# Kernel optimization log

Measured on AMD Instinct MI355X. Metric: run time of the kernel, lower is better.

## Reference

```python
import jax, jax.numpy as jnp
import numpy as np

BG_ID = 0
RADIUS = 10
MODE = 'gauss'
LAMBDA_B = 1.0
GAMMA = 0.1
TEMP = 4.0
EPS = 1e-8
BIG = 1e6  # stands in for +inf (no fg in a row/column); BIG**2 is fp32-safe


def setup_inputs() -> dict:
    key = jax.random.key(0)
    k1, k2 = jax.random.split(key)
    B, C, H, W = 4, 19, 256, 256
    return {
        'student_logits': jax.random.normal(k1, (B, C, H, W), jnp.float32),
        'teacher_logits': jax.random.normal(k2, (B, C, H, W), jnp.float32),
    }


def _edt2(fg):
    """Exact squared Euclidean distance transform of (1 - fg):
    distance from each pixel to the nearest foreground pixel.
    Separable algorithm: 1D column pass (two cumulative scans), then
    exact lower-envelope minimization along rows (vectorized brute force).
    fg: bool [B, H, W]. Returns float32 [B, H, W]."""
    B, H, W = fg.shape
    ii = jnp.arange(H, dtype=jnp.float32)[None, :, None]  # row index
    # 1D vertical distance to nearest fg pixel in each column
    d_fwd = ii - jax.lax.cummax(jnp.where(fg, ii, -BIG), axis=1)
    d_bwd = -jax.lax.cummax(jnp.where(fg, -ii, -BIG), axis=1, reverse=True) - ii
    g = jnp.minimum(jnp.minimum(d_fwd, d_bwd), BIG)  # [B,H,W]
    # exact 2D squared EDT: dist2[b,i,j] = min_{j'} (j-j')^2 + g[b,i,j']^2
    jj = jnp.arange(W, dtype=jnp.float32)
    diff2 = (jj[:, None] - jj[None, :]) ** 2  # [W, W']
    dist2 = jnp.min(diff2[None, None, :, :] + (g * g)[:, :, None, :], axis=-1)
    return dist2


def _erode(fg):
    """scipy.ndimage.binary_erosion with 4-connected cross structure and
    border_value=0 (out-of-bounds treated as background)."""
    p = jnp.pad(fg, ((0, 0), (1, 1), (1, 1)))
    return fg & p[:, :-2, 1:-1] & p[:, 2:, 1:-1] & p[:, 1:-1, :-2] & p[:, 1:-1, 2:]


def _weight_map(teacher_logits):
    # argmax of softmax(probs) == argmax of logits (softmax is monotone per-pixel)
    pred = jnp.argmax(teacher_logits, axis=1)  # [B,H,W]
    fg = pred != BG_ID
    dist2 = _edt2(fg)
    dist = jnp.sqrt(dist2)
    mask = (dist <= RADIUS).astype(jnp.float32)
    sigma = RADIUS / 2.0
    if MODE == 'gauss':
        wdist = jnp.exp(-dist2 / (2.0 * sigma * sigma))
    else:
        wdist = jnp.clip(1.0 - dist / RADIUS, 0.0, 1.0)
    wdist = wdist * mask
    boundary = (fg & ~_erode(fg)).astype(jnp.float32)
    # wb = wdist*(1+lambda_b*boundary); final weights = wb*mask_inside
    # (if an image has no fg pixels, dist is huge -> mask==0 -> weights==0,
    #  matching the scipy loop's `continue` which leaves zeros)
    return wdist * (1.0 + LAMBDA_B * boundary) * mask


def reference(student_logits, teacher_logits):
    weight_map = _weight_map(teacher_logits)  # [B,H,W]
    # teacher probs at temperature T (torch computes t_prob_T and t_prob
    # identically twice; computed once here)
    t_prob = jax.nn.softmax(teacher_logits / TEMP, axis=1)
    entropy = -jnp.sum(t_prob * jnp.log(jnp.clip(t_prob, EPS, None)), axis=1)
    ent_max = jnp.max(entropy, axis=(1, 2), keepdims=True)
    conf_factor = GAMMA + (1.0 - GAMMA) * (1.0 - entropy / (ent_max + EPS))
    s_logp = jax.nn.log_softmax(student_logits / TEMP, axis=1)
    kl_per_pixel = jnp.sum(t_prob * (jnp.log(t_prob + EPS) - s_logp), axis=1)
    total_weight = weight_map * conf_factor
    loss = jnp.sum(total_weight * kl_per_pixel) / (jnp.sum(total_weight) + EPS)
    return TEMP * TEMP * loss
```

## Files before the change

kernel.cpp:

```cpp
#include <hip/hip_runtime.h>
#include <math.h>

#define NC   19
#define HH   256
#define WW   256
#define NB   4
#define HW   (HH * WW)
#define NPIX (NB * HW)
#define RAD  10
#define CAP2 121.0f

__global__ __launch_bounds__(256) void k_pixel(
    const float* __restrict__ student, const float* __restrict__ teacher,
    float* __restrict__ entropy, float* __restrict__ kl,
    unsigned char* __restrict__ fg, float* __restrict__ bmax,
    double* __restrict__ acc, unsigned int* __restrict__ done)
{
    if (blockIdx.x == 0 && threadIdx.x == 0) {
        acc[0] = 0.0; acc[1] = 0.0; *done = 0u;
    }
    int q = (blockIdx.x * 256 + threadIdx.x) * 2;
    int b = q >> 16;
    int r = q & (HW - 1);
    const float* tb = teacher + (size_t)b * NC * HW + r;
    const float* sb = student + (size_t)b * NC * HW + r;

    float2 t[NC], s[NC];
    float tmx = -INFINITY, tmy = -INFINITY, smx = -INFINITY, smy = -INFINITY;
    int ax = 0, ay = 0;
#pragma unroll
    for (int c = 0; c < NC; ++c) {
        t[c] = *(const float2*)(tb + (size_t)c * HW);
        s[c] = *(const float2*)(sb + (size_t)c * HW);
        if (t[c].x > tmx) { tmx = t[c].x; ax = c; }
        if (t[c].y > tmy) { tmy = t[c].y; ay = c; }
        smx = fmaxf(smx, s[c].x);
        smy = fmaxf(smy, s[c].y);
    }
    float Stx = 0.f, Sty = 0.f, Ssx = 0.f, Ssy = 0.f;
    float T1x = 0.f, T1y = 0.f, T2x = 0.f, T2y = 0.f;
#pragma unroll
    for (int c = 0; c < NC; ++c) {
        float ex = __expf((t[c].x - tmx) * 0.25f);
        float ey = __expf((t[c].y - tmy) * 0.25f);
        Stx += ex;            Sty += ey;
        T1x += ex * t[c].x;   T1y += ey * t[c].y;
        T2x += ex * s[c].x;   T2y += ey * s[c].y;
        Ssx += __expf((s[c].x - smx) * 0.25f);
        Ssy += __expf((s[c].y - smy) * 0.25f);
    }
    float rStx = 1.0f / Stx, rSty = 1.0f / Sty;
    float entx = (tmx - T1x * rStx) * 0.25f + __logf(Stx);
    float enty = (tmy - T1y * rSty) * 0.25f + __logf(Sty);
    float klx = -entx - ((T2x * rStx - smx) * 0.25f - __logf(Ssx));
    float kly = -enty - ((T2y * rSty - smy) * 0.25f - __logf(Ssy));

    *(float2*)(entropy + q) = make_float2(entx, enty);
    *(float2*)(kl + q)      = make_float2(klx, kly);
    uchar2 fgv = make_uchar2((ax != 0) ? 1 : 0, (ay != 0) ? 1 : 0);
    *(uchar2*)(fg + q) = fgv;

    float m = fmaxf(entx, enty);
#pragma unroll
    for (int o = 32; o >= 1; o >>= 1) m = fmaxf(m, __shfl_down(m, o, 64));
    __shared__ float smem[4];
    int wave = threadIdx.x >> 6, lane = threadIdx.x & 63;
    if (lane == 0) smem[wave] = m;
    __syncthreads();
    if (threadIdx.x == 0)
        bmax[blockIdx.x] = fmaxf(fmaxf(smem[0], smem[1]), fmaxf(smem[2], smem[3]));
}

#define TS   32
#define HALO 10
#define FW   (TS + 2 * HALO)

__global__ __launch_bounds__(256) void k_tile(
    const unsigned char* __restrict__ fg, const float* __restrict__ entropy,
    const float* __restrict__ kl, const float* __restrict__ bmax,
    double* __restrict__ acc, unsigned int* __restrict__ done,
    float* __restrict__ out)
{
    __shared__ float fgt[FW][FW];
    __shared__ float vm[TS][FW];
    __shared__ float wmax[4];
    int b   = blockIdx.z;
    int ti0 = blockIdx.y * TS;
    int tj0 = blockIdx.x * TS;
    int tid = threadIdx.x;
    int wave = tid >> 6, lane = tid & 63;
    const unsigned char* fgb = fg + (size_t)b * HW;

    float m = bmax[b * 128 + (tid & 127)];
#pragma unroll
    for (int o = 32; o >= 1; o >>= 1) m = fmaxf(m, __shfl_down(m, o, 64));
    if (lane == 0) wmax[wave] = m;

    for (int l = tid; l < FW * FW; l += 256) {
        int li = l / FW, lj = l - li * FW;
        int gi = ti0 - HALO + li, gj = tj0 - HALO + lj;
        float v = 0.f;
        if (gi >= 0 && gi < HH && gj >= 0 && gj < WW) v = (float)fgb[gi * WW + gj];
        fgt[li][lj] = v;
    }
    __syncthreads();
    float em = fmaxf(fmaxf(wmax[0], wmax[1]), fmaxf(wmax[2], wmax[3]));

    for (int l = tid; l < TS * FW; l += 256) {
        int i = l / FW, j = l - i * FW;
        float mn = CAP2;
#pragma unroll
        for (int di = -HALO; di <= HALO; ++di) {
            float fv = fgt[i + HALO + di][j];
            mn = fminf(mn, (float)(di * di) + (1.0f - fv) * 1000.0f);
        }
        vm[i][j] = mn;
    }
    __syncthreads();

    double num = 0.0, den = 0.0;
#pragma unroll
    for (int k = 0; k < (TS * TS) / 256; ++k) {
        int p = tid + k * 256;
        int i = p >> 5, j = p & (TS - 1);
        float d2 = CAP2;
#pragma unroll
        for (int dj = -HALO; dj <= HALO; ++dj)
            d2 = fminf(d2, (float)(dj * dj) + vm[i][j + HALO + dj]);
        float mask  = (d2 <= 100.0f) ? 1.0f : 0.0f;
        float wdist = __expf(-d2 * 0.02f) * mask;

        float f  = fgt[i + HALO][j + HALO];
        float mn4 = fminf(fminf(fgt[i + HALO - 1][j + HALO], fgt[i + HALO + 1][j + HALO]),
                          fminf(fgt[i + HALO][j + HALO - 1], fgt[i + HALO][j + HALO + 1]));
        float boundary = (f != 0.f && mn4 == 0.f) ? 1.0f : 0.0f;

        float w = wdist * (1.0f + boundary) * mask;
        size_t gidx = (size_t)b * HW + (size_t)(ti0 + i) * WW + (tj0 + j);
        float conf = 0.1f + 0.9f * (1.0f - entropy[gidx] / (em + 1e-8f));
        float tw = w * conf;
        num += (double)(tw * kl[gidx]);
        den += (double)tw;
    }

#pragma unroll
    for (int o = 32; o >= 1; o >>= 1) {
        num += __shfl_down(num, o, 64);
        den += __shfl_down(den, o, 64);
    }
    __shared__ double snum[4], sden[4];
    if (lane == 0) { snum[wave] = num; sden[wave] = den; }
    __syncthreads();
    if (tid == 0) {
        atomicAdd(acc + 0, snum[0] + snum[1] + snum[2] + snum[3]);
        atomicAdd(acc + 1, sden[0] + sden[1] + sden[2] + sden[3]);
        __threadfence();
        unsigned int old = atomicAdd(done, 1u);
        if (old == (gridDim.x * gridDim.y * gridDim.z - 1)) {
            double tn = atomicAdd(acc + 0, 0.0);
            double td = atomicAdd(acc + 1, 0.0);
            out[0] = (float)(16.0 * tn / (td + 1e-8));
        }
    }
}

extern "C" void kernel_launch(void* const* d_in, const int* in_sizes, int n_in,
                              void* d_out, int out_size, void* d_ws, size_t ws_size,
                              hipStream_t stream)
{
    const float* student = (const float*)d_in[0];
    const float* teacher = (const float*)d_in[1];
    float* out = (float*)d_out;

    char* ws = (char*)d_ws;
    double*        acc     = (double*)(ws + 0);
    unsigned int*  done    = (unsigned int*)(ws + 16);
    float*         bmax    = (float*)(ws + 64);
    float*         entropy = (float*)(ws + 4096);
    float*         kl      = (float*)(ws + 4096 + (size_t)NPIX * 4);
    unsigned char* fg      = (unsigned char*)(ws + 4096 + (size_t)NPIX * 8);

    k_pixel<<<NPIX / 2 / 256, 256, 0, stream>>>(student, teacher, entropy, kl,
                                                fg, bmax, acc, done);
    dim3 g2(WW / TS, HH / TS, NB);
    k_tile<<<g2, 256, 0, stream>>>(fg, entropy, kl, bmax, acc, done, out);
}
```

Measured before the change: 94.21 us.

## Fuse pixel and tile kernels with grid-wide barrier, keep entropy/KL in registers

Merges the per-pixel softmax/KL pass and the distance-transform/weighting pass into one persistent kernel of 512 blocks. Each block owns two image rows and crosses a software grid barrier on an atomic counter. Entropy and KL stay in registers instead of going to global memory, so the intermediate write and read-back and one launch are removed. The cost is a spin barrier that needs all 512 blocks resident at once, plus an extra memset launch to reset the counters. Each block also reloads a 24-row halo of fg for only two rows of output.

New measurement: 145.9 us. 54.9% more time.

```diff
diff --git a/kernel.cpp b/kernel.cpp
--- a/kernel.cpp
+++ b/kernel.cpp
@@ -7,23 +7,31 @@
 #define NB   4
 #define HW   (HH * WW)
 #define NPIX (NB * HW)
-#define RAD  10
+#define NBLK 512
 #define CAP2 121.0f
 
-__global__ __launch_bounds__(256) void k_pixel(
+__global__ __launch_bounds__(256, 2) void k_fused(
     const float* __restrict__ student, const float* __restrict__ teacher,
-    float* __restrict__ entropy, float* __restrict__ kl,
     unsigned char* __restrict__ fg, float* __restrict__ bmax,
-    double* __restrict__ acc, unsigned int* __restrict__ done)
+    double* __restrict__ acc, unsigned int* __restrict__ sync_ctr,
+    unsigned int* __restrict__ done, float* __restrict__ out)
 {
-    if (blockIdx.x == 0 && threadIdx.x == 0) {
-        acc[0] = 0.0; acc[1] = 0.0; *done = 0u;
-    }
-    int q = (blockIdx.x * 256 + threadIdx.x) * 2;
-    int b = q >> 16;
-    int r = q & (HW - 1);
-    const float* tb = teacher + (size_t)b * NC * HW + r;
-    const float* sb = student + (size_t)b * NC * HW + r;
+    __shared__ float  fgt[24][WW];
+    __shared__ float  vm[2][276];
+    __shared__ float  red[4];
+    __shared__ double snum[4], sden[4];
+
+    const int tid  = threadIdx.x;
+    const int gb   = blockIdx.x;
+    const int b    = gb >> 7;
+    const int row0 = (gb & 127) * 2;
+    const int i_rel = tid >> 7;
+    const int j0   = (tid * 2) & 255;
+    const int wave = tid >> 6, lane = tid & 63;
+
+    const size_t base = (size_t)b * NC * HW + (size_t)(row0 + i_rel) * WW + j0;
+    const float* tb = teacher + base;
+    const float* sb = student + base;
 
     float2 t[NC], s[NC];
     float tmx = -INFINITY, tmy = -INFINITY, smx = -INFINITY, smy = -INFINITY;
@@ -55,91 +63,85 @@
     float klx = -entx - ((T2x * rStx - smx) * 0.25f - __logf(Ssx));
     float kly = -enty - ((T2y * rSty - smy) * 0.25f - __logf(Ssy));
 
-    *(float2*)(entropy + q) = make_float2(entx, enty);
-    *(float2*)(kl + q)      = make_float2(klx, kly);
-    uchar2 fgv = make_uchar2((ax != 0) ? 1 : 0, (ay != 0) ? 1 : 0);
-    *(uchar2*)(fg + q) = fgv;
+    const size_t gp = (size_t)b * HW + (size_t)(row0 + i_rel) * WW + j0;
+    *(uchar2*)(fg + gp) = make_uchar2((ax != 0) ? 1 : 0, (ay != 0) ? 1 : 0);
 
     float m = fmaxf(entx, enty);
 #pragma unroll
     for (int o = 32; o >= 1; o >>= 1) m = fmaxf(m, __shfl_down(m, o, 64));
-    __shared__ float smem[4];
-    int wave = threadIdx.x >> 6, lane = threadIdx.x & 63;
-    if (lane == 0) smem[wave] = m;
+    if (lane == 0) red[wave] = m;
     __syncthreads();
-    if (threadIdx.x == 0)
-        bmax[blockIdx.x] = fmaxf(fmaxf(smem[0], smem[1]), fmaxf(smem[2], smem[3]));
-}
+    if (tid == 0)
+        bmax[gb] = fmaxf(fmaxf(red[0], red[1]), fmaxf(red[2], red[3]));
 
-#define TS   32
-#define HALO 10
-#define FW   (TS + 2 * HALO)
-
-__global__ __launch_bounds__(256) void k_tile(
-    const unsigned char* __restrict__ fg, const float* __restrict__ entropy,
-    const float* __restrict__ kl, const float* __restrict__ bmax,
-    double* __restrict__ acc, unsigned int* __restrict__ done,
-    float* __restrict__ out)
-{
-    __shared__ float fgt[FW][FW];
-    __shared__ float vm[TS][FW];
-    __shared__ float wmax[4];
-    int b   = blockIdx.z;
-    int ti0 = blockIdx.y * TS;
-    int tj0 = blockIdx.x * TS;
-    int tid = threadIdx.x;
-    int wave = tid >> 6, lane = tid & 63;
-    const unsigned char* fgb = fg + (size_t)b * HW;
-
-    float m = bmax[b * 128 + (tid & 127)];
-#pragma unroll
-    for (int o = 32; o >= 1; o >>= 1) m = fmaxf(m, __shfl_down(m, o, 64));
-    if (lane == 0) wmax[wave] = m;
-
-    for (int l = tid; l < FW * FW; l += 256) {
-        int li = l / FW, lj = l - li * FW;
-        int gi = ti0 - HALO + li, gj = tj0 - HALO + lj;
-        float v = 0.f;
-        if (gi >= 0 && gi < HH && gj >= 0 && gj < WW) v = (float)fgb[gi * WW + gj];
-        fgt[li][lj] = v;
+    __syncthreads();
+    if (tid == 0) {
+        __hip_atomic_fetch_add(sync_ctr, 1u, __ATOMIC_RELEASE,
+                               __HIP_MEMORY_SCOPE_AGENT);
+        while (__hip_atomic_load(sync_ctr, __ATOMIC_ACQUIRE,
+                                 __HIP_MEMORY_SCOPE_AGENT) < NBLK)
+            __builtin_amdgcn_s_sleep(2);
+        __threadfence();
     }
     __syncthreads();
-    float em = fmaxf(fmaxf(wmax[0], wmax[1]), fmaxf(wmax[2], wmax[3]));
 
-    for (int l = tid; l < TS * FW; l += 256) {
-        int i = l / FW, j = l - i * FW;
+    float mm = bmax[(b << 7) + (tid & 127)];
+#pragma unroll
+    for (int o = 32; o >= 1; o >>= 1) mm = fmaxf(mm, __shfl_down(mm, o, 64));
+    if (lane == 0) red[wave] = mm;
+
+    const unsigned int* fgw = (const unsigned int*)(fg + (size_t)b * HW);
+    for (int l = tid; l < 24 * 64; l += 256) {
+        int r = l >> 6, c4 = (l & 63) * 4;
+        int grow = row0 - 11 + r;
+        unsigned int v = (grow >= 0 && grow < HH) ? fgw[grow * 64 + (l & 63)] : 0u;
+        fgt[r][c4 + 0] = (float)(v & 0xffu);
+        fgt[r][c4 + 1] = (float)((v >> 8) & 0xffu);
+        fgt[r][c4 + 2] = (float)((v >> 16) & 0xffu);
+        fgt[r][c4 + 3] = (float)((v >> 24) & 0xffu);
+    }
+    __syncthreads();
+    float em = fmaxf(fmaxf(red[0], red[1]), fmaxf(red[2], red[3]));
+
+    for (int l = tid; l < 2 * 276; l += 256) {
+        int i = l / 276, jj = l - i * 276;
+        int col = jj - 10;
         float mn = CAP2;
+        if (col >= 0 && col < WW) {
 #pragma unroll
-        for (int di = -HALO; di <= HALO; ++di) {
-            float fv = fgt[i + HALO + di][j];
-            mn = fminf(mn, (float)(di * di) + (1.0f - fv) * 1000.0f);
+            for (int di = -10; di <= 10; ++di) {
+                float fv = fgt[11 + i + di][col];
+                mn = fminf(mn, (float)(di * di) + (1.0f - fv) * 1000.0f);
+            }
         }
-        vm[i][j] = mn;
+        vm[i][jj] = mn;
     }
     __syncthreads();
 
     double num = 0.0, den = 0.0;
+    float entv[2] = {entx, enty}, klv[2] = {klx, kly};
 #pragma unroll
-    for (int k = 0; k < (TS * TS) / 256; ++k) {
-        int p = tid + k * 256;
-        int i = p >> 5, j = p & (TS - 1);
+    for (int k = 0; k < 2; ++k) {
+        int j = j0 + k;
         float d2 = CAP2;
 #pragma unroll
-        for (int dj = -HALO; dj <= HALO; ++dj)
-            d2 = fminf(d2, (float)(dj * dj) + vm[i][j + HALO + dj]);
+        for (int dj = -10; dj <= 10; ++dj)
+            d2 = fminf(d2, (float)(dj * dj) + vm[i_rel][j + dj + 10]);
         float mask  = (d2 <= 100.0f) ? 1.0f : 0.0f;
         float wdist = __expf(-d2 * 0.02f) * mask;
 
-        float f  = fgt[i + HALO][j + HALO];
-        float mn4 = fminf(fminf(fgt[i + HALO - 1][j + HALO], fgt[i + HALO + 1][j + HALO]),
-                          fminf(fgt[i + HALO][j + HALO - 1], fgt[i + HALO][j + HALO + 1]));
+        float f  = fgt[11 + i_rel][j];
+        float up = fgt[10 + i_rel][j];
+        float dn = fgt[12 + i_rel][j];
+        float lf = (j > 0)      ? fgt[11 + i_rel][j - 1] : 0.f;
+        float rt = (j < WW - 1) ? fgt[11 + i_rel][j + 1] : 0.f;
+        float mn4 = fminf(fminf(up, dn), fminf(lf, rt));
         float boundary = (f != 0.f && mn4 == 0.f) ? 1.0f : 0.0f;
 
         float w = wdist * (1.0f + boundary) * mask;
-        size_t gidx = (size_t)b * HW + (size_t)(ti0 + i) * WW + (tj0 + j);
-        float conf = 0.1f + 0.9f * (1.0f - entropy[gidx] / (em + 1e-8f));
+        float conf = 0.1f + 0.9f * (1.0f - entv[k] / (em + 1e-8f));
         float tw = w * conf;
-        num += (double)(tw * kl[gidx]);
+        num += (double)(tw * klv[k]);
         den += (double)tw;
     }
 
@@ -148,7 +150,6 @@
         num += __shfl_down(num, o, 64);
         den += __shfl_down(den, o, 64);
     }
-    __shared__ double snum[4], sden[4];
     if (lane == 0) { snum[wave] = num; sden[wave] = den; }
     __syncthreads();
     if (tid == 0) {
@@ -156,7 +157,7 @@
         atomicAdd(acc + 1, sden[0] + sden[1] + sden[2] + sden[3]);
         __threadfence();
         unsigned int old = atomicAdd(done, 1u);
-        if (old == (gridDim.x * gridDim.y * gridDim.z - 1)) {
+        if (old == NBLK - 1) {
             double tn = atomicAdd(acc + 0, 0.0);
             double td = atomicAdd(acc + 1, 0.0);
             out[0] = (float)(16.0 * tn / (td + 1e-8));
@@ -173,15 +174,14 @@
     float* out = (float*)d_out;
 
     char* ws = (char*)d_ws;
-    double*        acc     = (double*)(ws + 0);
-    unsigned int*  done    = (unsigned int*)(ws + 16);
-    float*         bmax    = (float*)(ws + 64);
-    float*         entropy = (float*)(ws + 4096);
-    float*         kl      = (float*)(ws + 4096 + (size_t)NPIX * 4);
-    unsigned char* fg      = (unsigned char*)(ws + 4096 + (size_t)NPIX * 8);
+    double*        acc      = (double*)(ws + 0);
+    unsigned int*  sync_ctr = (unsigned int*)(ws + 16);
+    unsigned int*  done     = (unsigned int*)(ws + 20);
+    float*         bmax     = (float*)(ws + 64);
+    unsigned char* fg       = (unsigned char*)(ws + 4096);
 
-    k_pixel<<<NPIX / 2 / 256, 256, 0, stream>>>(student, teacher, entropy, kl,
-                                                fg, bmax, acc, done);
-    dim3 g2(WW / TS, HH / TS, NB);
-    k_tile<<<g2, 256, 0, stream>>>(fg, entropy, kl, bmax, acc, done, out);
+    hipMemsetAsync(ws, 0, 64, stream);
+
+    k_fused<<<NBLK, 256, 0, stream>>>(student, teacher, fg, bmax,
+                                      acc, sync_ctr, done, out);
 }
```
